# Optimization experiments

Measured on AMD Instinct MI355X. Metric: run time of the kernel, lower is better.

## Reference

```python
import jax, jax.numpy as jnp
import numpy as np

N_NODES = 100000
N_EDGES = 1600000
NUM_FEATURES = 128
DIMS = [(NUM_FEATURES, 50), (50, 50), (50, 30), (30, 30), (30, 10), (10, 10), (10, 1)]


def setup_inputs() -> dict:
    key = jax.random.key(0)
    ks = jax.random.split(key, 4 + 2 * len(DIMS))
    inp = {
        "x": jax.random.normal(ks[0], (N_NODES, NUM_FEATURES), dtype=jnp.float32),
        "edge_index": jax.random.randint(ks[1], (2, N_EDGES), 0, N_NODES, dtype=jnp.int64) if jax.config.read("jax_enable_x64") else jax.random.randint(ks[1], (2, N_EDGES), 0, N_NODES, dtype=jnp.int32),
        "edge_weight": jax.random.uniform(ks[2], (N_EDGES,), dtype=jnp.float32),
    }
    for i, (fi, fo) in enumerate(DIMS):
        scale = 1.0 / np.sqrt(fi)
        inp[f"W{i+1}"] = jax.random.normal(ks[3 + 2 * i], (fi, fo), dtype=jnp.float32) * scale
        inp[f"b{i+1}"] = jax.random.normal(ks[4 + 2 * i], (fo,), dtype=jnp.float32) * 0.01
    return inp


def _gcn_norm(edge_index, edge_weight, n):
    # Add self-loops with weight 1, then symmetric normalization (PyG GCNConv).
    loops = jnp.arange(n)
    row = jnp.concatenate([edge_index[0], loops])
    col = jnp.concatenate([edge_index[1], loops])
    w = jnp.concatenate([edge_weight, jnp.ones((n,), edge_weight.dtype)])
    deg = jnp.zeros((n,), edge_weight.dtype).at[col].add(w)
    dinv = jnp.where(deg > 0, 1.0 / jnp.sqrt(deg), 0.0)
    norm = dinv[row] * w * dinv[col]
    return row, col, norm


def _gcn_conv(x, row, col, norm, W, b):
    h = x @ W                                # [N, out]
    msg = h[row] * norm[:, None]             # gather + edge scale [E+N, out]
    out = jnp.zeros_like(h).at[col].add(msg) # scatter-add
    return out + b


def _forward(x, edge_index, edge_weight, params):
    n = x.shape[0]
    row, col, norm = _gcn_norm(edge_index, edge_weight, n)  # shared across layers
    h = x
    n_layers = len(params)
    for i, (W, b) in enumerate(params):
        h = _gcn_conv(h, row, col, norm, W, b)
        if i < n_layers - 1:
            h = jax.nn.relu(h)
        # F.dropout treated as identity (eval mode) for a deterministic reference
    return h


def reference(x, edge_index, edge_weight, W1, b1, W2, b2, W3, b3, W4, b4, W5, b5, W6, b6, W7, b7):
    params = [(W1, b1), (W2, b2), (W3, b3), (W4, b4), (W5, b5), (W6, b6), (W7, b7)]
    return _forward(x, edge_index, edge_weight, params)
```

## Files before the change

kernel.cpp:

```cpp
#include <hip/hip_runtime.h>
#include <hip/hip_fp16.h>


static constexpr int NN = 100000;
static constexpr int NE = 1600000;
static constexpr int BKL = 9;
static constexpr int NBUK = (NN + 511) >> BKL;
static constexpr int EPT = 8;
static constexpr int EB = (NE + 2047) / 2048;


__global__ __launch_bounds__(256) void k_hist0(const int* __restrict__ col,
                                               int* __restrict__ counts) {
    __shared__ int lh[NBUK];
    for (int j = threadIdx.x; j < NBUK; j += 256) lh[j] = 0;
    __syncthreads();
    int base = blockIdx.x * 2048;
#pragma unroll
    for (int k = 0; k < EPT; ++k) {
        int e = base + k * 256 + threadIdx.x;
        if (e < NE) atomicAdd(&lh[col[e] >> BKL], 1);
    }
    __syncthreads();
    for (int j = threadIdx.x; j < NBUK; j += 256)
        counts[j * EB + blockIdx.x] = lh[j];
}


__global__ __launch_bounds__(256) void k_scanA(int* __restrict__ counts,
                                               int* __restrict__ btot) {
    __shared__ int lds[256];
    const int b = blockIdx.x;
    const int t = threadIdx.x;
    int* c = counts + (size_t)b * EB;
    constexpr int PER = (EB + 255) / 256;
    int v[PER];
    int s = 0;
#pragma unroll
    for (int k = 0; k < PER; ++k) {
        int idx = t * PER + k;
        v[k] = (idx < EB) ? c[idx] : 0;
        s += v[k];
    }
    lds[t] = s;
    __syncthreads();
    for (int off = 1; off < 256; off <<= 1) {
        int u = (t >= off) ? lds[t - off] : 0;
        __syncthreads();
        lds[t] += u;
        __syncthreads();
    }
    int run = lds[t] - s;
#pragma unroll
    for (int k = 0; k < PER; ++k) {
        int idx = t * PER + k;
        if (idx < EB) { c[idx] = run; run += v[k]; }
    }
    if (t == 255) btot[b] = lds[255];
}


__global__ void k_scanB(const int* __restrict__ btot, int* __restrict__ bstart) {
    __shared__ int lds[256];
    int t = threadIdx.x;
    int v = (t < NBUK) ? btot[t] : 0;
    lds[t] = v;
    __syncthreads();
    for (int off = 1; off < 256; off <<= 1) {
        int u = (t >= off) ? lds[t - off] : 0;
        __syncthreads();
        lds[t] += u;
        __syncthreads();
    }
    if (t < NBUK) bstart[t] = lds[t] - v;
    if (t == 0) bstart[NBUK] = NE;
}


__global__ __launch_bounds__(256) void k_A1(const int* __restrict__ row,
                                            const int* __restrict__ col,
                                            const float* __restrict__ ew,
                                            const int* __restrict__ counts,
                                            const int* __restrict__ bstart,
                                            int2* __restrict__ stg) {
    __shared__ int cur[NBUK];
    for (int j = threadIdx.x; j < NBUK; j += 256)
        cur[j] = bstart[j] + counts[j * EB + blockIdx.x];
    __syncthreads();
    int base = blockIdx.x * 2048;
#pragma unroll
    for (int k = 0; k < EPT; ++k) {
        int e = base + k * 256 + threadIdx.x;
        if (e < NE) {
            int c = col[e], r = row[e];
            int pos = atomicAdd(&cur[c >> BKL], 1);
            stg[pos] = make_int2(((c & 511) << 17) | r, __float_as_int(ew[e]));
        }
    }
}


__global__ __launch_bounds__(256) void k_bdeg(const int* __restrict__ bstart,
                                              const int2* __restrict__ stg,
                                              float* __restrict__ dinv) {
    __shared__ float sdeg[512];
    const int b = blockIdx.x;
    for (int j = threadIdx.x; j < 512; j += 256) sdeg[j] = 0.0f;
    __syncthreads();
    const int s = bstart[b], e = bstart[b + 1];
    for (int p = s + threadIdx.x; p < e; p += 256) {
        int2 rec = stg[p];
        atomicAdd(&sdeg[rec.x >> 17], __int_as_float(rec.y));
    }
    __syncthreads();
    for (int j = threadIdx.x; j < 512; j += 256) {
        int idx = (b << BKL) + j;
        if (idx < NN) dinv[idx] = rsqrtf(sdeg[j] + 1.0f);
    }
}


__global__ __launch_bounds__(512) void k_place(const int* __restrict__ bstart,
                                               const int2* __restrict__ stg,
                                               const float* __restrict__ dinv,
                                               int* __restrict__ offs,
                                               int2* __restrict__ csw) {
    __shared__ int lcnt[512];
    __shared__ int cur[512];
    const int b = blockIdx.x;
    const int t = threadIdx.x;
    lcnt[t] = 0;
    __syncthreads();
    const int s = bstart[b], e = bstart[b + 1];
    for (int p = s + t; p < e; p += 512)
        atomicAdd(&lcnt[stg[p].x >> 17], 1);
    __syncthreads();
    int v = lcnt[t];
    for (int off = 1; off < 512; off <<= 1) {
        int u = (t >= off) ? lcnt[t - off] : 0;
        __syncthreads();
        lcnt[t] += u;
        __syncthreads();
    }
    int excl = lcnt[t] - v;
    int idx = (b << BKL) + t;
    if (idx <= NN) offs[idx] = s + excl;
    cur[t] = s + excl;
    __syncthreads();
    for (int p = s + t; p < e; p += 512) {
        int2 rec = stg[p];
        int cl = rec.x >> 17;
        int r = rec.x & 0x1FFFF;
        float nw = dinv[r] * __int_as_float(rec.y) * dinv[(b << BKL) + cl];
        int slot = atomicAdd(&cur[cl], 1);
        csw[slot] = make_int2(r, __float_as_int(nw));
    }
}


typedef short s16x8 __attribute__((ext_vector_type(8)));
typedef short s16x4 __attribute__((ext_vector_type(4)));
typedef short s16x2 __attribute__((ext_vector_type(2)));
typedef float f32x4v __attribute__((ext_vector_type(4)));

static __device__ __forceinline__ unsigned short bf16rn(float f) {
    unsigned u = __float_as_uint(f);
    return (unsigned short)((u + 0x7FFFu + ((u >> 16) & 1u)) >> 16);
}

#define SWZ(r, k) ((k) ^ (((r) & 7) << 3))

__global__ __launch_bounds__(256) void k_matmul_f(const float* __restrict__ X,
                                                  const float* __restrict__ W,
                                                  __half* __restrict__ H) {
    __shared__ short lds[4 * 64 * 128];
    constexpr int XH = 0, XL = 8192, WHo = 16384, WLo = 24576;
    const int t = threadIdx.x;
    const int blk = blockIdx.x;

    {
        const int g = t & 31;
        const int rs = t >> 5;
#pragma unroll
        for (int i = 0; i < 8; ++i) {
            const int r = rs + 8 * i;
            const int row = blk * 64 + r;
            float4 v = make_float4(0.f, 0.f, 0.f, 0.f);
            if (row < NN) v = *(const float4*)(X + (size_t)row * 128 + g * 4);
            const float* vf = (const float*)&v;
            short h[4], l[4];
#pragma unroll
            for (int e = 0; e < 4; ++e) {
                unsigned short hb = bf16rn(vf[e]);
                float hf = __uint_as_float((unsigned)hb << 16);
                h[e] = (short)hb;
                l[e] = (short)bf16rn(vf[e] - hf);
            }
            const int k0 = SWZ(r, 4 * g);
            *(s16x4*)&lds[XH + r * 128 + k0] = *(const s16x4*)h;
            *(s16x4*)&lds[XL + r * 128 + k0] = *(const s16x4*)l;
        }
    }
    {
        const int c = t & 63;
        const int kq = t >> 6;
#pragma unroll
        for (int i = 0; i < 32; i += 2) {
            const int k = kq * 32 + i;
            float w0 = 0.f, w1 = 0.f;
            if (c < 50) { w0 = W[k * 50 + c]; w1 = W[(k + 1) * 50 + c]; }
            unsigned short h0 = bf16rn(w0), h1 = bf16rn(w1);
            float f0 = __uint_as_float((unsigned)h0 << 16);
            float f1 = __uint_as_float((unsigned)h1 << 16);
            short hh[2] = {(short)h0, (short)h1};
            short ll[2] = {(short)bf16rn(w0 - f0), (short)bf16rn(w1 - f1)};
            const int k0 = SWZ(c, k);
            *(s16x2*)&lds[WHo + c * 128 + k0] = *(const s16x2*)hh;
            *(s16x2*)&lds[WLo + c * 128 + k0] = *(const s16x2*)ll;
        }
    }
    __syncthreads();

    const int w = t >> 6;
    const int lane = t & 63;
    const int lr = lane & 15;
    const int kg = lane >> 4;
    const int ar = 16 * w + lr;
    f32x4v acc[4];
#pragma unroll
    for (int ct = 0; ct < 4; ++ct) acc[ct] = (f32x4v){0.f, 0.f, 0.f, 0.f};

#pragma unroll
    for (int kb = 0; kb < 4; ++kb) {
        const int kf = kb * 32 + kg * 8;
        const int ka = SWZ(ar, kf);
        s16x8 ah = *(const s16x8*)&lds[XH + ar * 128 + ka];
        s16x8 al = *(const s16x8*)&lds[XL + ar * 128 + ka];
        s16x8 bh[4], bl[4];
#pragma unroll
        for (int ct = 0; ct < 4; ++ct) {
            const int bc = ct * 16 + lr;
            const int kbo = SWZ(bc, kf);
            bh[ct] = *(const s16x8*)&lds[WHo + bc * 128 + kbo];
            bl[ct] = *(const s16x8*)&lds[WLo + bc * 128 + kbo];
        }
#pragma unroll
        for (int ct = 0; ct < 4; ++ct)
            acc[ct] = __builtin_amdgcn_mfma_f32_16x16x32_bf16(ah, bh[ct], acc[ct], 0, 0, 0);
#pragma unroll
        for (int ct = 0; ct < 4; ++ct)
            acc[ct] = __builtin_amdgcn_mfma_f32_16x16x32_bf16(ah, bl[ct], acc[ct], 0, 0, 0);
#pragma unroll
        for (int ct = 0; ct < 4; ++ct)
            acc[ct] = __builtin_amdgcn_mfma_f32_16x16x32_bf16(al, bh[ct], acc[ct], 0, 0, 0);
    }

    const int gr = blk * 64 + 16 * w + kg * 4;
#pragma unroll
    for (int ct = 0; ct < 4; ++ct) {
        const int col = ct * 16 + lr;
        if (col < 50) {
#pragma unroll
            for (int rg = 0; rg < 4; ++rg) {
                const int row = gr + rg;
                if (row < NN)
                    H[(size_t)row * 64 + col] = __float2half_rn(acc[ct][rg]);
            }
        }
    }
}
#undef SWZ


template <int FIN, int SX, int FOUT, int S, int NSPL>
__global__ __launch_bounds__(256, 2) void k_matmul_h(const __half* __restrict__ X,
                                                     const float* __restrict__ W,
                                                     __half* __restrict__ H) {
    constexpr int FC = FOUT / NSPL;
    constexpr int NCH = (FIN + 7) / 8;
    const int node = blockIdx.x * 256 + threadIdx.x;
    const int ch = blockIdx.y;
    if (node >= NN) return;
    const __half* xr = X + (size_t)node * SX;
    int4 raw[NCH];
#pragma unroll
    for (int c = 0; c < NCH; ++c) raw[c] = *(const int4*)(xr + 8 * c);
    float acc[FC];
#pragma unroll
    for (int j = 0; j < FC; ++j) acc[j] = 0.0f;
#pragma unroll
    for (int c = 0; c < NCH; ++c) {
        const __half2* hp = (const __half2*)&raw[c];
        const int lim = (FIN - 8 * c < 8) ? FIN - 8 * c : 8;
#pragma unroll
        for (int kk = 0; kk < 8; ++kk) {
            if (kk < lim) {
                __half2 pair = hp[kk >> 1];
                float xv = (kk & 1) ? __high2float(pair) : __low2float(pair);
                const float* wrow = W + (8 * c + kk) * FOUT + ch * FC;
#pragma unroll
                for (int j = 0; j < FC; ++j) acc[j] = fmaf(xv, wrow[j], acc[j]);
            }
        }
    }
    __half* hr = H + (size_t)node * S + ch * FC;
#pragma unroll
    for (int j = 0; j < FC; ++j) hr[j] = __float2half_rn(acc[j]);
}

__global__ void k_matmul_1h(const __half* __restrict__ X, const float* __restrict__ W,
                            float* __restrict__ H) {
    int i = blockIdx.x * blockDim.x + threadIdx.x;
    if (i >= NN) return;
    const __half* xr = X + (size_t)i * 16;
    int4 r0 = *(const int4*)xr;
    __half2 r1 = *(const __half2*)(xr + 8);
    const __half2* hp = (const __half2*)&r0;
    float acc = 0.0f;
#pragma unroll
    for (int q = 0; q < 4; ++q) {
        acc = fmaf(__low2float(hp[q]), W[2 * q], acc);
        acc = fmaf(__high2float(hp[q]), W[2 * q + 1], acc);
    }
    acc = fmaf(__low2float(r1), W[8], acc);
    acc = fmaf(__high2float(r1), W[9], acc);
    H[i] = acc;
}


static __device__ __forceinline__ int2 nt_load2(const int2* p) {
    unsigned long long raw = __builtin_nontemporal_load((const unsigned long long*)p);
    return make_int2((int)(raw & 0xFFFFFFFFull), (int)(raw >> 32));
}

template <int F, int SH, int SA, int LPN, bool RELU>
__global__ __launch_bounds__(256) void k_agg2(const int* __restrict__ offs,
                                              const int2* __restrict__ csw,
                                              const __half2* __restrict__ H,
                                              const float* __restrict__ dinv,
                                              const float* __restrict__ b,
                                              __half* __restrict__ O) {
    constexpr int R = F / 2;
    int t = blockIdx.x * blockDim.x + threadIdx.x;
    int g = t / LPN;
    int f = t - g * LPN;
    if (g >= NN) return;
    const int q0 = 4 * f;
    if (q0 >= R) return;
    int p = offs[g];
    const int pe = offs[g + 1];
    const int pl = pe - 1;

    float2 acc[4];
#pragma unroll
    for (int c = 0; c < 4; ++c) acc[c] = make_float2(0.f, 0.f);

    for (; p < pe; p += 4) {
        int2 e[4];
#pragma unroll
        for (int i = 0; i < 4; ++i) e[i] = nt_load2(csw + min(p + i, pl));
        __half2 h[4][4];
#pragma unroll
        for (int i = 0; i < 4; ++i)
            *(int4*)h[i] = *(const int4*)(H + (size_t)e[i].x * SH + q0);
#pragma unroll
        for (int i = 0; i < 4; ++i) {
            float w = (p + i < pe) ? __int_as_float(e[i].y) : 0.0f;
#pragma unroll
            for (int c = 0; c < 4; ++c) {
                acc[c].x = fmaf(__low2float(h[i][c]), w, acc[c].x);
                acc[c].y = fmaf(__high2float(h[i][c]), w, acc[c].y);
            }
        }
    }

    float di = dinv[g];
    float d2 = di * di;
    __half2 hs[4];
    *(int4*)hs = *(const int4*)(H + (size_t)g * SH + q0);
    __half2* orow = (__half2*)(O + (size_t)g * SA) + q0;
#pragma unroll
    for (int c = 0; c < 4; ++c) {
        if (q0 + c < R) {
            float vx = acc[c].x + fmaf(__low2float(hs[c]), d2, b[2 * (q0 + c)]);
            float vy = acc[c].y + fmaf(__high2float(hs[c]), d2, b[2 * (q0 + c) + 1]);
            if (RELU) { vx = fmaxf(vx, 0.f); vy = fmaxf(vy, 0.f); }
            orow[c] = __floats2half2_rn(vx, vy);
        }
    }
}

__global__ void k_agg1(const int* __restrict__ offs, const int2* __restrict__ csw,
                       const float* __restrict__ H, const float* __restrict__ dinv,
                       const float* __restrict__ b, float* __restrict__ O) {
    int g = blockIdx.x * blockDim.x + threadIdx.x;
    if (g >= NN) return;
    int p = offs[g];
    const int pe = offs[g + 1];
    const int pl = pe - 1;
    float a0 = 0.f, a1 = 0.f, a2 = 0.f, a3 = 0.f;
    for (; p < pe; p += 4) {
        int2 e0 = nt_load2(csw + min(p, pl)),     e1 = nt_load2(csw + min(p + 1, pl));
        int2 e2 = nt_load2(csw + min(p + 2, pl)), e3 = nt_load2(csw + min(p + 3, pl));
        float w0 = (p < pe)     ? __int_as_float(e0.y) : 0.f;
        float w1 = (p + 1 < pe) ? __int_as_float(e1.y) : 0.f;
        float w2 = (p + 2 < pe) ? __int_as_float(e2.y) : 0.f;
        float w3 = (p + 3 < pe) ? __int_as_float(e3.y) : 0.f;
        a0 = fmaf(H[e0.x], w0, a0);
        a1 = fmaf(H[e1.x], w1, a1);
        a2 = fmaf(H[e2.x], w2, a2);
        a3 = fmaf(H[e3.x], w3, a3);
    }
    float di = dinv[g];
    O[g] = ((a0 + a1) + (a2 + a3)) + fmaf(H[g], di * di, b[0]);
}


static inline size_t alignup(size_t x) { return (x + 255) & ~(size_t)255; }

extern "C" void kernel_launch(void* const* d_in, const int* in_sizes, int n_in,
                              void* d_out, int out_size, void* d_ws, size_t ws_size,
                              hipStream_t stream) {
    const float* x  = (const float*)d_in[0];
    const int*   ei = (const int*)d_in[1];
    const float* ew = (const float*)d_in[2];
    const float* Wp[7];
    const float* Bp[7];
    for (int l = 0; l < 7; ++l) {
        Wp[l] = (const float*)d_in[3 + 2 * l];
        Bp[l] = (const float*)d_in[4 + 2 * l];
    }
    const int* row = ei;
    const int* col = ei + NE;

    char* ws = (char*)d_ws;
    float* dinv  = (float*)ws;  ws += alignup((size_t)NN * 4);
    char*  Hb    = ws;          ws += alignup((size_t)NN * 64 * 2);
    char*  Aa    = ws;          ws += alignup((size_t)NN * 64 * 2);
    char*  Ab    = ws;          ws += alignup((size_t)NN * 64 * 2);
    int*   offs  = (int*)ws;    ws += alignup((size_t)(NN + 1) * 4);
    int*   counts= (int*)ws;    ws += alignup((size_t)NBUK * EB * 4);
    int*   btot  = (int*)ws;    ws += alignup((size_t)NBUK * 4);
    int*   bstart= (int*)ws;    ws += alignup((size_t)(NBUK + 1) * 4);
    int2*  stg   = (int2*)ws;   ws += alignup((size_t)NE * 8);
    int2*  csw   = (int2*)ws;   ws += alignup((size_t)NE * 8);

    const int gN = (NN + 255) / 256;
    const int gM = (NN + 63) / 64;

    k_hist0<<<EB, 256, 0, stream>>>(col, counts);
    k_scanA<<<NBUK, 256, 0, stream>>>(counts, btot);
    k_scanB<<<1, 256, 0, stream>>>(btot, bstart);
    k_A1<<<EB, 256, 0, stream>>>(row, col, ew, counts, bstart, stg);
    k_bdeg<<<NBUK, 256, 0, stream>>>(bstart, stg, dinv);
    k_place<<<NBUK, 512, 0, stream>>>(bstart, stg, dinv, offs, csw);

#define AGG(FOUT, S, LPN, RELU, OUT, LIDX)                                                  \
    k_agg2<FOUT, (S) / 2, S, LPN, RELU>                                                     \
        <<<((size_t)NN * (LPN) + 255) / 256, 256, 0, stream>>>(                             \
            offs, csw, (const __half2*)Hb, dinv, Bp[LIDX], (__half*)(OUT))

    k_matmul_f<<<gM, 256, 0, stream>>>(x, Wp[0], (__half*)Hb);
    AGG(50, 64, 8, true, Aa, 0);
    k_matmul_h<50, 64, 50, 64, 2><<<dim3(gN, 2), 256, 0, stream>>>((const __half*)Aa, Wp[1], (__half*)Hb);
    AGG(50, 64, 8, true, Ab, 1);
    k_matmul_h<50, 64, 30, 32, 2><<<dim3(gN, 2), 256, 0, stream>>>((const __half*)Ab, Wp[2], (__half*)Hb);
    AGG(30, 32, 4, true, Aa, 2);
    k_matmul_h<30, 32, 30, 32, 2><<<dim3(gN, 2), 256, 0, stream>>>((const __half*)Aa, Wp[3], (__half*)Hb);
    AGG(30, 32, 4, true, Ab, 3);
    k_matmul_h<30, 32, 10, 16, 1><<<dim3(gN, 1), 256, 0, stream>>>((const __half*)Ab, Wp[4], (__half*)Hb);
    AGG(10, 16, 2, true, Aa, 4);
    k_matmul_h<10, 16, 10, 16, 1><<<dim3(gN, 1), 256, 0, stream>>>((const __half*)Aa, Wp[5], (__half*)Hb);
    AGG(10, 16, 2, true, Ab, 5);
#undef AGG

    k_matmul_1h<<<gN, 256, 0, stream>>>((const __half*)Ab, Wp[6], (float*)Hb);
    k_agg1<<<gN, 256, 0, stream>>>(offs, csw, (const float*)Hb, dinv, Bp[6],
                                   (float*)d_out);
}
```

Measured before the change: 479.9 us.

## Pre-split W1 into bf16 hi/lo once and load X directly into registers

```diff
diff --git a/kernel.cpp b/kernel.cpp
--- a/kernel.cpp
+++ b/kernel.cpp
@@ -159,8 +159,6 @@
 
 
 typedef short s16x8 __attribute__((ext_vector_type(8)));
-typedef short s16x4 __attribute__((ext_vector_type(4)));
-typedef short s16x2 __attribute__((ext_vector_type(2)));
 typedef float f32x4v __attribute__((ext_vector_type(4)));
 
 static __device__ __forceinline__ unsigned short bf16rn(float f) {
@@ -168,81 +166,74 @@
     return (unsigned short)((u + 0x7FFFu + ((u >> 16) & 1u)) >> 16);
 }
 
-#define SWZ(r, k) ((k) ^ (((r) & 7) << 3))
-
-__global__ __launch_bounds__(256) void k_matmul_f(const float* __restrict__ X,
-                                                  const float* __restrict__ W,
-                                                  __half* __restrict__ H) {
-    __shared__ short lds[4 * 64 * 128];
-    constexpr int XH = 0, XL = 8192, WHo = 16384, WLo = 24576;
+__global__ void k_wsplit(const float* __restrict__ W, short* __restrict__ wt) {
     const int t = threadIdx.x;
-    const int blk = blockIdx.x;
+#pragma unroll
+    for (int i = 0; i < 32; ++i) {
+        const int li = t + 256 * i;
+        const int c = li >> 7, k = li & 127;
+        float f = (c < 50) ? W[k * 50 + c] : 0.f;
+        unsigned short hb = bf16rn(f);
+        float hf = __uint_as_float((unsigned)hb << 16);
+        unsigned short lb = bf16rn(f - hf);
+        const int off = c * 128 + (k ^ ((c & 7) << 3));
+        wt[off] = (short)hb;
+        wt[8192 + off] = (short)lb;
+    }
+}
+
+__global__ __launch_bounds__(256, 4) void k_matmul_f(const float* __restrict__ X,
+                                                     const short* __restrict__ wt,
+                                                     __half* __restrict__ H) {
+    __shared__ short lds[2 * 64 * 128];
+    const int t = threadIdx.x;
 
     {
-        const int g = t & 31;
-        const int rs = t >> 5;
-#pragma unroll
-        for (int i = 0; i < 8; ++i) {
-            const int r = rs + 8 * i;
-            const int row = blk * 64 + r;
-            float4 v = make_float4(0.f, 0.f, 0.f, 0.f);
-            if (row < NN) v = *(const float4*)(X + (size_t)row * 128 + g * 4);
-            const float* vf = (const float*)&v;
-            short h[4], l[4];
-#pragma unroll
-            for (int e = 0; e < 4; ++e) {
-                unsigned short hb = bf16rn(vf[e]);
-                float hf = __uint_as_float((unsigned)hb << 16);
-                h[e] = (short)hb;
-                l[e] = (short)bf16rn(vf[e] - hf);
-            }
-            const int k0 = SWZ(r, 4 * g);
-            *(s16x4*)&lds[XH + r * 128 + k0] = *(const s16x4*)h;
-            *(s16x4*)&lds[XL + r * 128 + k0] = *(const s16x4*)l;
-        }
-    }
-    {
-        const int c = t & 63;
-        const int kq = t >> 6;
-#pragma unroll
-        for (int i = 0; i < 32; i += 2) {
-            const int k = kq * 32 + i;
-            float w0 = 0.f, w1 = 0.f;
-            if (c < 50) { w0 = W[k * 50 + c]; w1 = W[(k + 1) * 50 + c]; }
-            unsigned short h0 = bf16rn(w0), h1 = bf16rn(w1);
-            float f0 = __uint_as_float((unsigned)h0 << 16);
-            float f1 = __uint_as_float((unsigned)h1 << 16);
-            short hh[2] = {(short)h0, (short)h1};
-            short ll[2] = {(short)bf16rn(w0 - f0), (short)bf16rn(w1 - f1)};
-            const int k0 = SWZ(c, k);
-            *(s16x2*)&lds[WHo + c * 128 + k0] = *(const s16x2*)hh;
-            *(s16x2*)&lds[WLo + c * 128 + k0] = *(const s16x2*)ll;
-        }
-    }
-    __syncthreads();
+        const int4* src = (const int4*)wt;
+        int4* dst = (int4*)lds;
+#pragma unroll
+        for (int j = 0; j < 8; ++j) dst[j * 256 + t] = src[j * 256 + t];
+    }
 
     const int w = t >> 6;
     const int lane = t & 63;
     const int lr = lane & 15;
     const int kg = lane >> 4;
-    const int ar = 16 * w + lr;
+    const int row = blockIdx.x * 64 + 16 * w + lr;
+    const float* xr = X + (size_t)(row < NN ? row : NN - 1) * 128 + kg * 8;
+
+    float4 xa[4][2];
+#pragma unroll
+    for (int kb = 0; kb < 4; ++kb) {
+        xa[kb][0] = *(const float4*)(xr + kb * 32);
+        xa[kb][1] = *(const float4*)(xr + kb * 32 + 4);
+    }
+
+    __syncthreads();
+
     f32x4v acc[4];
 #pragma unroll
     for (int ct = 0; ct < 4; ++ct) acc[ct] = (f32x4v){0.f, 0.f, 0.f, 0.f};
 
 #pragma unroll
     for (int kb = 0; kb < 4; ++kb) {
+        s16x8 ah, al;
+        const unsigned* xu = (const unsigned*)&xa[kb][0];
+#pragma unroll
+        for (int e = 0; e < 8; ++e) {
+            const unsigned u = xu[e];
+            const float lo = __uint_as_float(u) - __uint_as_float(u & 0xFFFF0000u);
+            ah[e] = (short)(u >> 16);
+            al[e] = (short)(__float_as_uint(lo) >> 16);
+        }
         const int kf = kb * 32 + kg * 8;
-        const int ka = SWZ(ar, kf);
-        s16x8 ah = *(const s16x8*)&lds[XH + ar * 128 + ka];
-        s16x8 al = *(const s16x8*)&lds[XL + ar * 128 + ka];
         s16x8 bh[4], bl[4];
 #pragma unroll
         for (int ct = 0; ct < 4; ++ct) {
             const int bc = ct * 16 + lr;
-            const int kbo = SWZ(bc, kf);
-            bh[ct] = *(const s16x8*)&lds[WHo + bc * 128 + kbo];
-            bl[ct] = *(const s16x8*)&lds[WLo + bc * 128 + kbo];
+            const int ko = bc * 128 + (kf ^ ((bc & 7) << 3));
+            bh[ct] = *(const s16x8*)&lds[ko];
+            bl[ct] = *(const s16x8*)&lds[8192 + ko];
         }
 #pragma unroll
         for (int ct = 0; ct < 4; ++ct)
@@ -255,21 +246,20 @@
             acc[ct] = __builtin_amdgcn_mfma_f32_16x16x32_bf16(al, bh[ct], acc[ct], 0, 0, 0);
     }
 
-    const int gr = blk * 64 + 16 * w + kg * 4;
+    const int gr = blockIdx.x * 64 + 16 * w + kg * 4;
 #pragma unroll
     for (int ct = 0; ct < 4; ++ct) {
         const int col = ct * 16 + lr;
         if (col < 50) {
 #pragma unroll
             for (int rg = 0; rg < 4; ++rg) {
-                const int row = gr + rg;
-                if (row < NN)
-                    H[(size_t)row * 64 + col] = __float2half_rn(acc[ct][rg]);
+                const int orow = gr + rg;
+                if (orow < NN)
+                    H[(size_t)orow * 64 + col] = __float2half_rn(acc[ct][rg]);
             }
         }
     }
 }
-#undef SWZ
 
 
 template <int FIN, int SX, int FOUT, int S, int NSPL>
@@ -444,10 +434,12 @@
     int*   bstart= (int*)ws;    ws += alignup((size_t)(NBUK + 1) * 4);
     int2*  stg   = (int2*)ws;   ws += alignup((size_t)NE * 8);
     int2*  csw   = (int2*)ws;   ws += alignup((size_t)NE * 8);
+    short* wt    = (short*)ws;  ws += alignup((size_t)2 * 64 * 128 * 2);
 
     const int gN = (NN + 255) / 256;
     const int gM = (NN + 63) / 64;
 
+    k_wsplit<<<1, 256, 0, stream>>>(Wp[0], wt);
     k_hist0<<<EB, 256, 0, stream>>>(col, counts);
     k_scanA<<<NBUK, 256, 0, stream>>>(counts, btot);
     k_scanB<<<1, 256, 0, stream>>>(btot, bstart);
@@ -460,7 +452,7 @@
         <<<((size_t)NN * (LPN) + 255) / 256, 256, 0, stream>>>(                             \
             offs, csw, (const __half2*)Hb, dinv, Bp[LIDX], (__half*)(OUT))
 
-    k_matmul_f<<<gM, 256, 0, stream>>>(x, Wp[0], (__half*)Hb);
+    k_matmul_f<<<gM, 256, 0, stream>>>(x, wt, (__half*)Hb);
     AGG(50, 64, 8, true, Aa, 0);
     k_matmul_h<50, 64, 50, 64, 2><<<dim3(gN, 2), 256, 0, stream>>>((const __half*)Aa, Wp[1], (__half*)Hb);
     AGG(50, 64, 8, true, Ab, 1);
```

After: 457.7 us. -4.6%, faster.
